# Optimization experiments

Measured on AMD Instinct MI355X. Metric: run time of the kernel, lower is better.

## Reference

```python
import jax, jax.numpy as jnp
import numpy as np

jax.config.update("jax_enable_x64", True)

TOL = 1e-06


def setup_inputs() -> dict:
    key = jax.random.key(0)
    k1, k2 = jax.random.split(key)
    n, d = 4096, 128
    output = jax.random.normal(k1, (n, d), dtype=jnp.float32)
    # target: square roots of patristic distances -> nonnegative
    target = jax.random.uniform(k2, (n, n), dtype=jnp.float32) * 2.0
    return {"output": output, "target": target}


def reference(output, target):
    # Torch module casts to double before all math
    out = output.astype(jnp.float64)
    tgt = target.astype(jnp.float64)
    n = out.shape[0]

    # Lorentz inner product: B = outer(s, s) - out @ out.T, s = sqrt(1 + ||o||^2)
    s = jnp.sqrt(1.0 + jnp.sum(out * out, axis=1))          # [n]
    B = s[:, None] * s[None, :] - out @ out.T               # [n, n]

    # Clamp near-1 entries exactly to 1 (torch: B[(B-1).abs() < tol] = 1.0)
    clamp = jnp.abs(B - 1.0) < TOL
    # Safe acosh: evaluate at 2.0 where clamped to avoid inf/nan, then set dist=0 there
    B_safe = jnp.where(clamp, 2.0, B)
    dist = jnp.where(clamp, 0.0, jnp.arccosh(B_safe))       # acosh(1) == 0

    # Strictly-lower-triangular masked MAE
    tril_mask = jnp.tril(jnp.ones((n, n), dtype=jnp.float64), k=-1)
    loss = jnp.sum(jnp.abs(dist - tgt) * tril_mask) / (n * (n - 1))
    return loss
```

## Files before the change

### kernel.cpp

```cpp
#include <hip/hip_runtime.h>
#include <math.h>

#define N 4096
#define D 128
#define TS 64
#define NT (N / TS)
#define NBLK (NT * (NT + 1) / 2)
#define NG (N / 16)

typedef __attribute__((ext_vector_type(8))) short short8;
typedef __attribute__((ext_vector_type(4))) float f32x4;

union frag_u { short8 v; unsigned int u[4]; };

__device__ __forceinline__ unsigned int pack_bf16x2(float a, float b) {
    unsigned int ua = __float_as_uint(a), ub = __float_as_uint(b);
    ua = (ua + 0x7FFFu + ((ua >> 16) & 1u)) >> 16;
    ub = (ub + 0x7FFFu + ((ub >> 16) & 1u)) >> 16;
    return ua | (ub << 16);
}

__global__ __launch_bounds__(256)
void prep_kernel(const float* __restrict__ O,
                 short8* __restrict__ Ofrag,
                 float* __restrict__ s) {
    __shared__ float psum[16][17];
    const int g    = blockIdx.x;
    const int tid  = threadIdx.x;
    const int kk   = tid >> 6;
    const int lane = tid & 63;
    const int r16  = lane & 15;
    const int qd   = lane >> 4;
    const float* src = O + (size_t)(g * 16 + r16) * D + kk * 32 + qd * 8;
    const float4 v0 = *(const float4*)(src);
    const float4 v1 = *(const float4*)(src + 4);
    frag_u f;
    f.u[0] = pack_bf16x2(v0.x, v0.y);
    f.u[1] = pack_bf16x2(v0.z, v0.w);
    f.u[2] = pack_bf16x2(v1.x, v1.y);
    f.u[3] = pack_bf16x2(v1.z, v1.w);
    Ofrag[(g * 4 + kk) * 64 + lane] = f.v;
    psum[kk * 4 + qd][r16] = v0.x * v0.x + v0.y * v0.y + v0.z * v0.z + v0.w * v0.w
                           + v1.x * v1.x + v1.y * v1.y + v1.z * v1.z + v1.w * v1.w;
    __syncthreads();
    if (tid < 16) {
        float acc = 1.0f;
        #pragma unroll
        for (int x = 0; x < 16; x++) acc += psum[x][tid];
        s[g * 16 + tid] = sqrtf(acc);
    }
}

__device__ __forceinline__ float acosh_dist(float B) {
    if (fabsf(B - 1.0f) < 1e-6f) return 0.0f;
    const float Bc = fmaxf(B, 1.0f);
    return __log2f(Bc + sqrtf(fmaf(Bc, Bc, -1.0f))) * 0.6931471805599453f;
}

__device__ __forceinline__ void gload_lds16(const float* g, float* l) {
    __builtin_amdgcn_global_load_lds(
        (const __attribute__((address_space(1))) unsigned int*)g,
        (__attribute__((address_space(3))) unsigned int*)l,
        16, 0, 0);
}

__global__ __launch_bounds__(256, 4)
void tile_loss_kernel(const short8* __restrict__ Fr,
                      const float* __restrict__ s,
                      const float* __restrict__ tgt,
                      float* __restrict__ partials) {
    __shared__ float T[TS][TS];
    __shared__ float wsum[4];

    const int t = blockIdx.x;
    int ti = (int)((sqrtf(8.0f * (float)t + 1.0f) - 1.0f) * 0.5f);
    while ((ti + 1) * (ti + 2) / 2 <= t) ti++;
    while (ti * (ti + 1) / 2 > t) ti--;
    const int tj = t - ti * (ti + 1) / 2;

    const int tid  = threadIdx.x;
    const int wave = tid >> 6;
    const int lane = tid & 63;
    const int quad = lane >> 4;
    const int l16  = lane & 15;

    const int ib0 = ti * TS;
    const int jb  = tj * TS;
    const int r0  = wave * 16 + quad * 4;

    const int ga4 = (ti * 4 + wave) * 4;
    const int gb4 = tj * 4 * 4;
    short8 a[4], b[4][4];
    #pragma unroll
    for (int k = 0; k < 4; k++) a[k] = Fr[(ga4 + k) * 64 + lane];
    #pragma unroll
    for (int n = 0; n < 4; n++)
        #pragma unroll
        for (int k = 0; k < 4; k++) b[n][k] = Fr[(gb4 + n * 4 + k) * 64 + lane];

    float sj[4];
    #pragma unroll
    for (int n = 0; n < 4; n++) sj[n] = s[jb + n * 16 + l16];
    float si[4];
    #pragma unroll
    for (int r = 0; r < 4; r++) si[r] = s[ib0 + r0 + r];

    {
        const float* gsrc = tgt + (size_t)(ib0 + wave * 16 + (lane >> 4)) * N
                          + jb + (lane & 15) * 4;
        #pragma unroll
        for (int q = 0; q < 4; q++)
            gload_lds16(gsrc + (size_t)q * 4 * N, &T[wave * 16 + q * 4][0]);
    }

    f32x4 acc[4] = {};
    #pragma unroll
    for (int k = 0; k < 4; k++)
        #pragma unroll
        for (int n = 0; n < 4; n++)
            acc[n] = __builtin_amdgcn_mfma_f32_16x16x32_bf16(a[k], b[n][k], acc[n], 0, 0, 0);

    asm volatile("s_waitcnt vmcnt(0)" ::: "memory");
    __syncthreads();

    float lsum = 0.0f;
    if (ti != tj) {
        #pragma unroll
        for (int r = 0; r < 4; r++)
            #pragma unroll
            for (int n = 0; n < 4; n++) {
                const float B  = fmaf(si[r], sj[n], -acc[n][r]);
                const float tv = T[r0 + r][n * 16 + l16];
                lsum += fabsf(acosh_dist(B) - tv);
            }
    } else {
        #pragma unroll
        for (int r = 0; r < 4; r++) {
            const int i = ib0 + r0 + r;
            #pragma unroll
            for (int n = 0; n < 4; n++) {
                const int j = jb + n * 16 + l16;
                if (j < i) {
                    const float B  = fmaf(si[r], sj[n], -acc[n][r]);
                    const float tv = T[r0 + r][n * 16 + l16];
                    lsum += fabsf(acosh_dist(B) - tv);
                }
            }
        }
    }

    #pragma unroll
    for (int off = 32; off > 0; off >>= 1)
        lsum += __shfl_down(lsum, off, 64);
    if (lane == 0) wsum[wave] = lsum;
    __syncthreads();
    if (tid == 0)
        partials[t] = wsum[0] + wsum[1] + wsum[2] + wsum[3];
}

__global__ __launch_bounds__(256)
void final_reduce_kernel(const float* __restrict__ partials,
                         float* __restrict__ loss) {
    __shared__ float wsum[4];
    const int tid  = threadIdx.x;
    const int wave = tid >> 6;
    const int lane = tid & 63;
    float acc = 0.0f;
    for (int i = tid; i < NBLK; i += 256) acc += partials[i];
    #pragma unroll
    for (int off = 32; off > 0; off >>= 1)
        acc += __shfl_down(acc, off, 64);
    if (lane == 0) wsum[wave] = acc;
    __syncthreads();
    if (tid == 0) {
        const float tot = wsum[0] + wsum[1] + wsum[2] + wsum[3];
        loss[0] = tot * (1.0f / ((float)N * (float)(N - 1)));
    }
}

extern "C" void kernel_launch(void* const* d_in, const int* in_sizes, int n_in,
                              void* d_out, int out_size, void* d_ws, size_t ws_size,
                              hipStream_t stream) {
    const float* O   = (const float*)d_in[0];
    const float* tgt = (const float*)d_in[1];
    float* loss = (float*)d_out;

    short8* Ofrag = (short8*)d_ws;
    float* s        = (float*)((char*)d_ws + (size_t)N * D * 2);
    float* partials = s + N;

    prep_kernel<<<NG, 256, 0, stream>>>(O, Ofrag, s);
    tile_loss_kernel<<<NBLK, 256, 0, stream>>>(Ofrag, s, tgt, partials);
    final_reduce_kernel<<<1, 256, 0, stream>>>(partials, loss);
}
```

Before: 103.3 us.

## Process two triangular tiles per block with prefetched target loads overlapping compute

Each block now handles two lower-triangle tiles (t and t+NBLK/2), issuing the second tile's target loads into a second LDS buffer before the first tile's MFMA and epilogue, then waiting with a partial vmcnt. The aim is to hide global load latency for the target matrix and to halve the block count and per-block launch overhead. The cost is doubled LDS use, more live registers and fewer blocks for latency hiding. The partial waitcnt count of 16 also assumes a particular order for the outstanding loads, which is fragile.

Result: slower. 124.7 us (+20.7%).

```diff
diff --git a/kernel.cpp b/kernel.cpp
--- a/kernel.cpp
+++ b/kernel.cpp
@@ -6,6 +6,7 @@
 #define TS 64
 #define NT (N / TS)
 #define NBLK (NT * (NT + 1) / 2)
+#define HBLK (NBLK / 2)
 #define NG (N / 16)
 
 typedef __attribute__((ext_vector_type(8))) short short8;
@@ -64,54 +65,92 @@
         16, 0, 0);
 }
 
+__device__ __forceinline__ void tile_ij(int t, int& ti_, int& tj_) {
+    int x = (int)((sqrtf(8.0f * (float)t + 1.0f) - 1.0f) * 0.5f);
+    while ((x + 1) * (x + 2) / 2 <= t) x++;
+    while (x * (x + 1) / 2 > t) x--;
+    ti_ = x;
+    tj_ = t - x * (x + 1) / 2;
+}
+
+__device__ __forceinline__ float tile_epilogue(const f32x4 acc[4],
+                                               const float si[4], const float sj[4],
+                                               const float (*Tt)[TS],
+                                               int r0, int l16, int ib0, int jb,
+                                               int diag) {
+    float lsum = 0.0f;
+    if (!diag) {
+        #pragma unroll
+        for (int r = 0; r < 4; r++)
+            #pragma unroll
+            for (int n = 0; n < 4; n++) {
+                const float B = fmaf(si[r], sj[n], -acc[n][r]);
+                lsum += fabsf(acosh_dist(B) - Tt[r0 + r][n * 16 + l16]);
+            }
+    } else {
+        #pragma unroll
+        for (int r = 0; r < 4; r++) {
+            const int i = ib0 + r0 + r;
+            #pragma unroll
+            for (int n = 0; n < 4; n++) {
+                const int j = jb + n * 16 + l16;
+                if (j < i)
+                    lsum += fabsf(acosh_dist(fmaf(si[r], sj[n], -acc[n][r]))
+                                  - Tt[r0 + r][n * 16 + l16]);
+            }
+        }
+    }
+    return lsum;
+}
+
 __global__ __launch_bounds__(256, 4)
 void tile_loss_kernel(const short8* __restrict__ Fr,
                       const float* __restrict__ s,
                       const float* __restrict__ tgt,
                       float* __restrict__ partials) {
-    __shared__ float T[TS][TS];
-    __shared__ float wsum[4];
-
-    const int t = blockIdx.x;
-    int ti = (int)((sqrtf(8.0f * (float)t + 1.0f) - 1.0f) * 0.5f);
-    while ((ti + 1) * (ti + 2) / 2 <= t) ti++;
-    while (ti * (ti + 1) / 2 > t) ti--;
-    const int tj = t - ti * (ti + 1) / 2;
+    __shared__ float T[2][TS][TS];
+    __shared__ float wsum[2][4];
 
     const int tid  = threadIdx.x;
     const int wave = tid >> 6;
     const int lane = tid & 63;
     const int quad = lane >> 4;
     const int l16  = lane & 15;
-
-    const int ib0 = ti * TS;
-    const int jb  = tj * TS;
-    const int r0  = wave * 16 + quad * 4;
-
-    const int ga4 = (ti * 4 + wave) * 4;
-    const int gb4 = tj * 4 * 4;
+    const int r0   = wave * 16 + quad * 4;
+
+    const int tA = blockIdx.x;
+    const int tB = tA + HBLK;
+    int tiA, tjA, tiB, tjB;
+    tile_ij(tA, tiA, tjA);
+    tile_ij(tB, tiB, tjB);
+    const int ibA = tiA * TS, jbA = tjA * TS;
+    const int ibB = tiB * TS, jbB = tjB * TS;
+
+    {
+        const float* g = tgt + (size_t)(ibA + wave * 16 + quad) * N + jbA + l16 * 4;
+        #pragma unroll
+        for (int q = 0; q < 4; q++)
+            gload_lds16(g + (size_t)q * 4 * N, &T[0][wave * 16 + q * 4][0]);
+    }
+
     short8 a[4], b[4][4];
     #pragma unroll
-    for (int k = 0; k < 4; k++) a[k] = Fr[(ga4 + k) * 64 + lane];
+    for (int k = 0; k < 4; k++)
+        a[k] = Fr[((tiA * 4 + wave) * 4 + k) * 64 + lane];
     #pragma unroll
     for (int n = 0; n < 4; n++)
         #pragma unroll
-        for (int k = 0; k < 4; k++) b[n][k] = Fr[(gb4 + n * 4 + k) * 64 + lane];
-
-    float sj[4];
-    #pragma unroll
-    for (int n = 0; n < 4; n++) sj[n] = s[jb + n * 16 + l16];
-    float si[4];
-    #pragma unroll
-    for (int r = 0; r < 4; r++) si[r] = s[ib0 + r0 + r];
-
+        for (int k = 0; k < 4; k++)
+            b[n][k] = Fr[((tjA * 4 + n) * 4 + k) * 64 + lane];
+
+    __builtin_amdgcn_sched_barrier(0);
     {
-        const float* gsrc = tgt + (size_t)(ib0 + wave * 16 + (lane >> 4)) * N
-                          + jb + (lane & 15) * 4;
+        const float* g = tgt + (size_t)(ibB + wave * 16 + quad) * N + jbB + l16 * 4;
         #pragma unroll
         for (int q = 0; q < 4; q++)
-            gload_lds16(gsrc + (size_t)q * 4 * N, &T[wave * 16 + q * 4][0]);
-    }
+            gload_lds16(g + (size_t)q * 4 * N, &T[1][wave * 16 + q * 4][0]);
+    }
+    __builtin_amdgcn_sched_barrier(0);
 
     f32x4 acc[4] = {};
     #pragma unroll
@@ -120,42 +159,57 @@
         for (int n = 0; n < 4; n++)
             acc[n] = __builtin_amdgcn_mfma_f32_16x16x32_bf16(a[k], b[n][k], acc[n], 0, 0, 0);
 
-    asm volatile("s_waitcnt vmcnt(0)" ::: "memory");
-    __syncthreads();
-
-    float lsum = 0.0f;
-    if (ti != tj) {
-        #pragma unroll
-        for (int r = 0; r < 4; r++)
-            #pragma unroll
-            for (int n = 0; n < 4; n++) {
-                const float B  = fmaf(si[r], sj[n], -acc[n][r]);
-                const float tv = T[r0 + r][n * 16 + l16];
-                lsum += fabsf(acosh_dist(B) - tv);
-            }
-    } else {
-        #pragma unroll
-        for (int r = 0; r < 4; r++) {
-            const int i = ib0 + r0 + r;
-            #pragma unroll
-            for (int n = 0; n < 4; n++) {
-                const int j = jb + n * 16 + l16;
-                if (j < i) {
-                    const float B  = fmaf(si[r], sj[n], -acc[n][r]);
-                    const float tv = T[r0 + r][n * 16 + l16];
-                    lsum += fabsf(acosh_dist(B) - tv);
-                }
-            }
-        }
-    }
-
+    asm volatile("s_waitcnt vmcnt(16)" ::: "memory");
+    __builtin_amdgcn_s_barrier();
+
+    #pragma unroll
+    for (int k = 0; k < 4; k++)
+        a[k] = Fr[((tiB * 4 + wave) * 4 + k) * 64 + lane];
+    #pragma unroll
+    for (int n = 0; n < 4; n++)
+        #pragma unroll
+        for (int k = 0; k < 4; k++)
+            b[n][k] = Fr[((tjB * 4 + n) * 4 + k) * 64 + lane];
+    float siA[4], sjA[4], siB[4], sjB[4];
+    #pragma unroll
+    for (int r = 0; r < 4; r++) siA[r] = s[ibA + r0 + r];
+    #pragma unroll
+    for (int n = 0; n < 4; n++) sjA[n] = s[jbA + n * 16 + l16];
+    #pragma unroll
+    for (int r = 0; r < 4; r++) siB[r] = s[ibB + r0 + r];
+    #pragma unroll
+    for (int n = 0; n < 4; n++) sjB[n] = s[jbB + n * 16 + l16];
+
+    float lsum = tile_epilogue(acc, siA, sjA, T[0], r0, l16, ibA, jbA, tiA == tjA);
     #pragma unroll
     for (int off = 32; off > 0; off >>= 1)
         lsum += __shfl_down(lsum, off, 64);
-    if (lane == 0) wsum[wave] = lsum;
-    __syncthreads();
+    if (lane == 0) wsum[0][wave] = lsum;
+    asm volatile("s_waitcnt lgkmcnt(0)" ::: "memory");
+    __builtin_amdgcn_s_barrier();
     if (tid == 0)
-        partials[t] = wsum[0] + wsum[1] + wsum[2] + wsum[3];
+        partials[tA] = wsum[0][0] + wsum[0][1] + wsum[0][2] + wsum[0][3];
+
+    #pragma unroll
+    for (int n = 0; n < 4; n++) acc[n] = (f32x4){0.0f, 0.0f, 0.0f, 0.0f};
+    #pragma unroll
+    for (int k = 0; k < 4; k++)
+        #pragma unroll
+        for (int n = 0; n < 4; n++)
+            acc[n] = __builtin_amdgcn_mfma_f32_16x16x32_bf16(a[k], b[n][k], acc[n], 0, 0, 0);
+
+    asm volatile("s_waitcnt vmcnt(0)" ::: "memory");
+    __builtin_amdgcn_s_barrier();
+
+    float lsumB = tile_epilogue(acc, siB, sjB, T[1], r0, l16, ibB, jbB, tiB == tjB);
+    #pragma unroll
+    for (int off = 32; off > 0; off >>= 1)
+        lsumB += __shfl_down(lsumB, off, 64);
+    if (lane == 0) wsum[1][wave] = lsumB;
+    asm volatile("s_waitcnt lgkmcnt(0)" ::: "memory");
+    __builtin_amdgcn_s_barrier();
+    if (tid == 0)
+        partials[tB] = wsum[1][0] + wsum[1][1] + wsum[1][2] + wsum[1][3];
 }
 
 __global__ __launch_bounds__(256)
@@ -190,6 +244,6 @@
     float* partials = s + N;
 
     prep_kernel<<<NG, 256, 0, stream>>>(O, Ofrag, s);
-    tile_loss_kernel<<<NBLK, 256, 0, stream>>>(Ofrag, s, tgt, partials);
+    tile_loss_kernel<<<HBLK, 256, 0, stream>>>(Ofrag, s, tgt, partials);
     final_reduce_kernel<<<1, 256, 0, stream>>>(partials, loss);
 }
```

## Enlarge loss tiles to 128x128 with per-wave 32-row MFMA blocks

Applied to the files above, without the earlier changes.

Doubles the triangular tile size so each block covers a 128x128 tile, and each wave computes two 16-row groups against eight column groups. A fragments are reused across twice as many columns, and the per-block count drops about fourfold, cutting launch and reduction overhead. The per-block LDS barrier is removed and per-wave partials are written directly. Accumulation moves to double precision. The cost is more registers and LDS (64KB) per block, lower occupancy, and coarser work for the diagonal tiles.

Measured after the change: 115.1 us. 1.11x slower.

```diff
diff --git a/kernel.cpp b/kernel.cpp
--- a/kernel.cpp
+++ b/kernel.cpp
@@ -3,7 +3,7 @@
 
 #define N 4096
 #define D 128
-#define TS 64
+#define TS 128
 #define NT (N / TS)
 #define NBLK (NT * (NT + 1) / 2)
 #define NG (N / 16)
@@ -64,19 +64,20 @@
         16, 0, 0);
 }
 
-__global__ __launch_bounds__(256, 4)
+__device__ __forceinline__ void tile_ij(int t, int& ti_, int& tj_) {
+    int x = (int)((sqrtf(8.0f * (float)t + 1.0f) - 1.0f) * 0.5f);
+    while ((x + 1) * (x + 2) / 2 <= t) x++;
+    while (x * (x + 1) / 2 > t) x--;
+    ti_ = x;
+    tj_ = t - x * (x + 1) / 2;
+}
+
+__global__ __launch_bounds__(256, 2)
 void tile_loss_kernel(const short8* __restrict__ Fr,
                       const float* __restrict__ s,
                       const float* __restrict__ tgt,
-                      float* __restrict__ partials) {
+                      float* __restrict__ wpart) {
     __shared__ float T[TS][TS];
-    __shared__ float wsum[4];
-
-    const int t = blockIdx.x;
-    int ti = (int)((sqrtf(8.0f * (float)t + 1.0f) - 1.0f) * 0.5f);
-    while ((ti + 1) * (ti + 2) / 2 <= t) ti++;
-    while (ti * (ti + 1) / 2 > t) ti--;
-    const int tj = t - ti * (ti + 1) / 2;
 
     const int tid  = threadIdx.x;
     const int wave = tid >> 6;
@@ -84,97 +85,112 @@
     const int quad = lane >> 4;
     const int l16  = lane & 15;
 
+    int ti, tj;
+    tile_ij(blockIdx.x, ti, tj);
     const int ib0 = ti * TS;
     const int jb  = tj * TS;
-    const int r0  = wave * 16 + quad * 4;
-
-    const int ga4 = (ti * 4 + wave) * 4;
-    const int gb4 = tj * 4 * 4;
-    short8 a[4], b[4][4];
-    #pragma unroll
-    for (int k = 0; k < 4; k++) a[k] = Fr[(ga4 + k) * 64 + lane];
-    #pragma unroll
-    for (int n = 0; n < 4; n++)
-        #pragma unroll
-        for (int k = 0; k < 4; k++) b[n][k] = Fr[(gb4 + n * 4 + k) * 64 + lane];
-
-    float sj[4];
-    #pragma unroll
-    for (int n = 0; n < 4; n++) sj[n] = s[jb + n * 16 + l16];
-    float si[4];
-    #pragma unroll
-    for (int r = 0; r < 4; r++) si[r] = s[ib0 + r0 + r];
 
     {
-        const float* gsrc = tgt + (size_t)(ib0 + wave * 16 + (lane >> 4)) * N
-                          + jb + (lane & 15) * 4;
-        #pragma unroll
-        for (int q = 0; q < 4; q++)
-            gload_lds16(gsrc + (size_t)q * 4 * N, &T[wave * 16 + q * 4][0]);
-    }
-
-    f32x4 acc[4] = {};
-    #pragma unroll
-    for (int k = 0; k < 4; k++)
+        const float* g = tgt + (size_t)(ib0 + wave * 32 + (lane >> 5)) * N
+                       + jb + (lane & 31) * 4;
+        #pragma unroll
+        for (int q = 0; q < 16; q++)
+            gload_lds16(g + (size_t)(2 * q) * N, &T[wave * 32 + 2 * q][0]);
+    }
+    __builtin_amdgcn_sched_barrier(0);
+
+    short8 a[2][4];
+    #pragma unroll
+    for (int rg = 0; rg < 2; rg++)
+        #pragma unroll
+        for (int k = 0; k < 4; k++)
+            a[rg][k] = Fr[((ti * 8 + wave * 2 + rg) * 4 + k) * 64 + lane];
+
+    const int rbase = wave * 32 + quad * 4;
+    float si[2][4], sj[8];
+    #pragma unroll
+    for (int rg = 0; rg < 2; rg++)
+        #pragma unroll
+        for (int r = 0; r < 4; r++)
+            si[rg][r] = s[ib0 + rbase + rg * 16 + r];
+    #pragma unroll
+    for (int n = 0; n < 8; n++) sj[n] = s[jb + n * 16 + l16];
+
+    f32x4 acc[2][8] = {};
+    #pragma unroll
+    for (int h = 0; h < 2; h++) {
+        short8 b[4][4];
         #pragma unroll
         for (int n = 0; n < 4; n++)
-            acc[n] = __builtin_amdgcn_mfma_f32_16x16x32_bf16(a[k], b[n][k], acc[n], 0, 0, 0);
+            #pragma unroll
+            for (int k = 0; k < 4; k++)
+                b[n][k] = Fr[((tj * 8 + h * 4 + n) * 4 + k) * 64 + lane];
+        #pragma unroll
+        for (int k = 0; k < 4; k++)
+            #pragma unroll
+            for (int n = 0; n < 4; n++)
+                #pragma unroll
+                for (int rg = 0; rg < 2; rg++)
+                    acc[rg][h * 4 + n] = __builtin_amdgcn_mfma_f32_16x16x32_bf16(
+                        a[rg][k], b[n][k], acc[rg][h * 4 + n], 0, 0, 0);
+        if (h == 0) __builtin_amdgcn_sched_barrier(0);
+    }
 
     asm volatile("s_waitcnt vmcnt(0)" ::: "memory");
-    __syncthreads();
-
-    float lsum = 0.0f;
+    __builtin_amdgcn_sched_barrier(0);
+
+    double lsum = 0.0;
     if (ti != tj) {
         #pragma unroll
-        for (int r = 0; r < 4; r++)
-            #pragma unroll
-            for (int n = 0; n < 4; n++) {
-                const float B  = fmaf(si[r], sj[n], -acc[n][r]);
-                const float tv = T[r0 + r][n * 16 + l16];
-                lsum += fabsf(acosh_dist(B) - tv);
-            }
+        for (int rg = 0; rg < 2; rg++)
+            #pragma unroll
+            for (int n = 0; n < 8; n++)
+                #pragma unroll
+                for (int r = 0; r < 4; r++) {
+                    const float B  = fmaf(si[rg][r], sj[n], -acc[rg][n][r]);
+                    const float tv = T[rbase + rg * 16 + r][n * 16 + l16];
+                    lsum += (double)fabsf(acosh_dist(B) - tv);
+                }
     } else {
         #pragma unroll
-        for (int r = 0; r < 4; r++) {
-            const int i = ib0 + r0 + r;
-            #pragma unroll
-            for (int n = 0; n < 4; n++) {
-                const int j = jb + n * 16 + l16;
-                if (j < i) {
-                    const float B  = fmaf(si[r], sj[n], -acc[n][r]);
-                    const float tv = T[r0 + r][n * 16 + l16];
-                    lsum += fabsf(acosh_dist(B) - tv);
+        for (int rg = 0; rg < 2; rg++)
+            #pragma unroll
+            for (int n = 0; n < 8; n++)
+                #pragma unroll
+                for (int r = 0; r < 4; r++) {
+                    const int i = ib0 + rbase + rg * 16 + r;
+                    const int j = jb + n * 16 + l16;
+                    if (j < i) {
+                        const float B  = fmaf(si[rg][r], sj[n], -acc[rg][n][r]);
+                        const float tv = T[rbase + rg * 16 + r][n * 16 + l16];
+                        lsum += (double)fabsf(acosh_dist(B) - tv);
+                    }
                 }
-            }
-        }
     }
 
     #pragma unroll
     for (int off = 32; off > 0; off >>= 1)
         lsum += __shfl_down(lsum, off, 64);
-    if (lane == 0) wsum[wave] = lsum;
-    __syncthreads();
-    if (tid == 0)
-        partials[t] = wsum[0] + wsum[1] + wsum[2] + wsum[3];
+    if (lane == 0) wpart[blockIdx.x * 4 + wave] = (float)lsum;
 }
 
 __global__ __launch_bounds__(256)
-void final_reduce_kernel(const float* __restrict__ partials,
+void final_reduce_kernel(const float* __restrict__ wpart,
                          float* __restrict__ loss) {
-    __shared__ float wsum[4];
+    __shared__ double wsum[4];
     const int tid  = threadIdx.x;
     const int wave = tid >> 6;
     const int lane = tid & 63;
-    float acc = 0.0f;
-    for (int i = tid; i < NBLK; i += 256) acc += partials[i];
+    double acc = 0.0;
+    for (int i = tid; i < NBLK * 4; i += 256) acc += (double)wpart[i];
     #pragma unroll
     for (int off = 32; off > 0; off >>= 1)
         acc += __shfl_down(acc, off, 64);
     if (lane == 0) wsum[wave] = acc;
     __syncthreads();
     if (tid == 0) {
-        const float tot = wsum[0] + wsum[1] + wsum[2] + wsum[3];
-        loss[0] = tot * (1.0f / ((float)N * (float)(N - 1)));
+        const double tot = ((wsum[0] + wsum[1]) + wsum[2]) + wsum[3];
+        loss[0] = (float)(tot * (1.0 / ((double)N * (double)(N - 1))));
     }
 }
 
@@ -186,10 +202,10 @@
     float* loss = (float*)d_out;
 
     short8* Ofrag = (short8*)d_ws;
-    float* s        = (float*)((char*)d_ws + (size_t)N * D * 2);
-    float* partials = s + N;
+    float* s      = (float*)((char*)d_ws + (size_t)N * D * 2);
+    float* wpart  = s + N;
 
     prep_kernel<<<NG, 256, 0, stream>>>(O, Ofrag, s);
-    tile_loss_kernel<<<NBLK, 256, 0, stream>>>(Ofrag, s, tgt, partials);
-    final_reduce_kernel<<<1, 256, 0, stream>>>(partials, loss);
-}
+    tile_loss_kernel<<<NBLK, 256, 0, stream>>>(Ofrag, s, tgt, wpart);
+    final_reduce_kernel<<<1, 256, 0, stream>>>(wpart, loss);
+}
```
